# Kernel tuning notes

Hardware: AMD Instinct MI355X
Metric: run time of the kernel (lower is better)

## Reference

```python
import jax, jax.numpy as jnp
import numpy as np

B, C, H, W = 8, 64, 128, 128
OC, KH, KW = 64, 3, 3
STRIDE, PAD, DIL = 1, 1, 1
DG = 1            # deformable groups
G = 1             # conv groups
K = KH * KW
HO = (H + 2 * PAD - DIL * (KH - 1) - 1) // STRIDE + 1
WO = (W + 2 * PAD - DIL * (KW - 1) - 1) // STRIDE + 1


def setup_inputs() -> dict:
    key = jax.random.key(0)
    k1, k2, k3, k4 = jax.random.split(key, 4)
    input_tensor = jax.random.normal(k1, (B, C, H, W), dtype=jnp.float32)
    offset = jax.random.normal(k2, (B, DG * 2 * K, HO, WO), dtype=jnp.float32)
    mask = jax.random.uniform(k3, (B, DG * K, HO, WO), dtype=jnp.float32)
    n = C * KH * KW
    std_v = 1.0 / np.sqrt(n)
    weight = jax.random.uniform(k4, (OC, C // G, KH, KW), dtype=jnp.float32,
                                minval=-std_v, maxval=std_v)
    bias = jnp.zeros((OC,), dtype=jnp.float32)
    return {"input_tensor": input_tensor, "offset": offset, "mask": mask,
            "weight": weight, "bias": bias}


def _bilinear_sample(img, py, px):
    # img: [Cg, H, W]; py, px: [K, HO, WO] fractional sample coords
    y0 = jnp.floor(py).astype(jnp.int32)
    x0 = jnp.floor(px).astype(jnp.int32)
    y1, x1 = y0 + 1, x0 + 1
    wy1 = py - y0.astype(py.dtype)
    wx1 = px - x0.astype(px.dtype)
    wy0, wx0 = 1.0 - wy1, 1.0 - wx1

    def gather(yy, xx):
        valid = ((yy >= 0) & (yy < H) & (xx >= 0) & (xx < W)).astype(img.dtype)
        yc = jnp.clip(yy, 0, H - 1)
        xc = jnp.clip(xx, 0, W - 1)
        return img[:, yc, xc] * valid  # [Cg, K, HO, WO], zero outside

    return (gather(y0, x0) * (wy0 * wx0) + gather(y0, x1) * (wy0 * wx1)
            + gather(y1, x0) * (wy1 * wx0) + gather(y1, x1) * (wy1 * wx1))


def _mdconv(input_tensor, offset, mask, weight, bias):
    Cg = C // DG
    ky = (jnp.arange(K) // KW).astype(jnp.float32)   # kernel row per tap
    kx = (jnp.arange(K) % KW).astype(jnp.float32)    # kernel col per tap
    oy = jnp.arange(HO, dtype=jnp.float32) * STRIDE - PAD
    ox = jnp.arange(WO, dtype=jnp.float32) * STRIDE - PAD
    base_y = ky[:, None] * DIL + oy[None, :]         # [K, HO]
    base_x = kx[:, None] * DIL + ox[None, :]         # [K, WO]

    off = offset.reshape(B, DG, K, 2, HO, WO)
    py = base_y[None, None, :, :, None] + off[:, :, :, 0]  # [B, DG, K, HO, WO]
    px = base_x[None, None, :, None, :] + off[:, :, :, 1]

    imgs = input_tensor.reshape(B, DG, Cg, H, W)
    sample = jax.vmap(jax.vmap(_bilinear_sample))           # over B then DG
    cols = sample(imgs, py, px)                             # [B, DG, Cg, K, HO, WO]
    cols = cols * mask.reshape(B, DG, 1, K, HO, WO)
    cols = cols.reshape(B, G, C // G, K, HO, WO)

    w = weight.reshape(G, OC // G, C // G, K)
    out = jnp.einsum('gock,bgckpq->bgopq', w, cols)
    out = out.reshape(B, OC, HO, WO) + bias[None, :, None, None]
    return out


def reference(input_tensor, offset, mask, weight, bias):
    return _mdconv(input_tensor, offset, mask, weight, bias)
```

## Files before the change

### kernel.cpp

```cpp
#include <hip/hip_runtime.h>
#include <stdint.h>

typedef unsigned short u16;

#define B_ 8
#define C_ 64
#define H_ 128
#define W_ 128
#define OC_ 64
#define HO_ 128
#define WO_ 128
#define HWC_ (H_*W_*C_)
#define PADW 72

typedef __attribute__((ext_vector_type(8))) short short8;
typedef __attribute__((ext_vector_type(4))) float f32x4;

__device__ __forceinline__ u16 f2bf(float f) {
  union { float f; uint32_t i; } v; v.f = f;
  uint32_t r = v.i + 0x7FFFu + ((v.i >> 16) & 1u);
  return (u16)(r >> 16);
}
__device__ __forceinline__ uint32_t pkbf(float lo, float hi) {
  uint32_t r;
  asm("v_cvt_pk_bf16_f32 %0, %1, %2" : "=v"(r) : "v"(lo), "v"(hi));
  return r;
}
#define BF_LO(u) __uint_as_float((uint32_t)(u) << 16)
#define BF_HI(u) __uint_as_float((uint32_t)(u) & 0xFFFF0000u)

__global__ void wprep_kernel(const float* __restrict__ w, u16* __restrict__ wk2) {
  const int idx = blockIdx.x * 256 + threadIdx.x;
  const int j    = idx & 7;
  const int lane = (idx >> 3) & 63;
  const int kk   = (idx >> 9) & 1;
  const int m    = (idx >> 10) & 1;
  const int wr   = (idx >> 11) & 1;
  const int k    = idx >> 12;
  const int oc = wr*32 + m*16 + (lane & 15);
  const int c  = kk*32 + (lane >> 4)*8 + j;
  wk2[idx] = f2bf(w[(oc*C_ + c)*9 + k]);
}

__global__ __launch_bounds__(256) void nhwc_kernel(const float* __restrict__ in,
                                                   u16* __restrict__ nhwc) {
  __shared__ float t[64][65];
  const int b = blockIdx.z, h = blockIdx.y, w0 = blockIdx.x * 64;
  const int tid = threadIdx.x;
  for (int idx = tid; idx < 64*64; idx += 256) {
    int c = idx >> 6, w = idx & 63;
    t[w][c] = in[((b*C_ + c)*H_ + h)*W_ + w0 + w];
  }
  __syncthreads();
  for (int idx = tid; idx < 64*64; idx += 256) {
    int w = idx >> 6, c = idx & 63;
    nhwc[((b*H_ + h)*W_ + w0 + w)*C_ + c] = f2bf(t[w][c]);
  }
}

__device__ __forceinline__ uint32_t blend1(uint32_t g00, uint32_t g01,
                                           uint32_t g10, uint32_t g11, float4 w) {
  float lo = w.x*BF_LO(g00) + w.y*BF_LO(g01) + w.z*BF_LO(g10) + w.w*BF_LO(g11);
  float hi = w.x*BF_HI(g00) + w.y*BF_HI(g01) + w.z*BF_HI(g10) + w.w*BF_HI(g11);
  return pkbf(lo, hi);
}

__global__ __launch_bounds__(256, 4) void mdconv_main(
    const float* __restrict__ offs, const float* __restrict__ mask,
    const float* __restrict__ bias, const u16* __restrict__ nhwc,
    const u16* __restrict__ wk2, float* __restrict__ out)
{
  __shared__ u16 clds[64*PADW];
  __shared__ int2 pA[576];
  __shared__ float4 pW[576];

  const int tid = threadIdx.x;
  const int lane = tid & 63;
  const int wv = tid >> 6;
  const int b = blockIdx.z;
  const int p = blockIdx.y;
  const int q0 = blockIdx.x * 64;

  for (int item = tid; item < 576; item += 256) {
    const int k = item >> 6;
    const int px = item & 63;
    const int q = q0 + px;
    const int ky = k / 3, kx = k % 3;
    const float oy = offs[((b*18 + 2*k)*HO_ + p)*WO_ + q];
    const float ox = offs[((b*18 + 2*k + 1)*HO_ + p)*WO_ + q];
    const float mm = mask[((b*9 + k)*HO_ + p)*WO_ + q];
    const float py  = (float)(ky + p - 1) + oy;
    const float pxx = (float)(kx + q - 1) + ox;
    const float y0f = floorf(py), x0f = floorf(pxx);
    const int y0 = (int)y0f, x0 = (int)x0f;
    const int y1 = y0 + 1, x1 = x0 + 1;
    const float wy1 = py - y0f, wx1 = pxx - x0f;
    const float wy0 = 1.f - wy1, wx0 = 1.f - wx1;
    const bool vy0 = (y0 >= 0) & (y0 < H_);
    const bool vy1 = (y1 >= 0) & (y1 < H_);
    const bool vx0 = (x0 >= 0) & (x0 < W_);
    const bool vx1 = (x1 >= 0) & (x1 < W_);
    const float w00 = (vy0 & vx0) ? wy0*wx0*mm : 0.f;
    const float w01 = (vy0 & vx1) ? wy0*wx1*mm : 0.f;
    const float w10 = (vy1 & vx0) ? wy1*wx0*mm : 0.f;
    const float w11 = (vy1 & vx1) ? wy1*wx1*mm : 0.f;
    const int y0c = min(max(y0,0),H_-1), y1c = min(max(y1,0),H_-1);
    const int x0c = min(max(x0,0),W_-1), x1c = min(max(x1,0),W_-1);
    const int dx = (x1c - x0c) * C_;
    const int dy = (y1c - y0c) * W_ * C_;
    pA[item] = make_int2(b*HWC_ + (y0c*W_ + x0c)*C_, dx | (dy << 16));
    pW[item] = make_float4(w00, w01, w10, w11);
  }
  __syncthreads();

  f32x4 acc00 = {0.f,0.f,0.f,0.f};
  f32x4 acc01 = acc00, acc10 = acc00, acc11 = acc00;
  const int wr = wv >> 1, wc = wv & 1;
  const u16* cb = &clds[(wc*32 + (lane & 15))*PADW + (lane >> 4)*8];
  const int px0 = tid >> 3;
  const int c8 = (tid & 7) * 8;

  for (int k = 0; k < 9; ++k) {
    const u16* wg = wk2 + (k*2 + wr)*2048 + lane*8;
    const short8 a00 = *(const short8*)(wg);
    const short8 a01 = *(const short8*)(wg + 512);
    const short8 a10 = *(const short8*)(wg + 1024);
    const short8 a11 = *(const short8*)(wg + 1536);

    {
      const int piA = k*64 + px0, piB = piA + 32;
      const int2 aA = pA[piA];
      const int2 aB = pA[piB];
      const float4 wA = pW[piA];
      const float4 wB = pW[piB];
      const u16* sA = nhwc + aA.x + c8;
      const u16* sB = nhwc + aB.x + c8;
      const int dxA = aA.y & 0xFFFF, dyA = ((uint32_t)aA.y) >> 16;
      const int dxB = aB.y & 0xFFFF, dyB = ((uint32_t)aB.y) >> 16;
      const uint4 gA00 = *(const uint4*)(sA);
      const uint4 gA01 = *(const uint4*)(sA + dxA);
      const uint4 gA10 = *(const uint4*)(sA + dyA);
      const uint4 gA11 = *(const uint4*)(sA + dyA + dxA);
      const uint4 gB00 = *(const uint4*)(sB);
      const uint4 gB01 = *(const uint4*)(sB + dxB);
      const uint4 gB10 = *(const uint4*)(sB + dyB);
      const uint4 gB11 = *(const uint4*)(sB + dyB + dxB);
      uint4 rA, rB;
      rA.x = blend1(gA00.x, gA01.x, gA10.x, gA11.x, wA);
      rA.y = blend1(gA00.y, gA01.y, gA10.y, gA11.y, wA);
      rA.z = blend1(gA00.z, gA01.z, gA10.z, gA11.z, wA);
      rA.w = blend1(gA00.w, gA01.w, gA10.w, gA11.w, wA);
      rB.x = blend1(gB00.x, gB01.x, gB10.x, gB11.x, wB);
      rB.y = blend1(gB00.y, gB01.y, gB10.y, gB11.y, wB);
      rB.z = blend1(gB00.z, gB01.z, gB10.z, gB11.z, wB);
      rB.w = blend1(gB00.w, gB01.w, gB10.w, gB11.w, wB);
      *(uint4*)(&clds[px0*PADW + c8]) = rA;
      *(uint4*)(&clds[(px0+32)*PADW + c8]) = rB;
    }
    __syncthreads();

    const short8 b00 = *(const short8*)(cb);
    const short8 b01 = *(const short8*)(cb + 32);
    const short8 b10 = *(const short8*)(cb + 16*PADW);
    const short8 b11 = *(const short8*)(cb + 16*PADW + 32);
    acc00 = __builtin_amdgcn_mfma_f32_16x16x32_bf16(a00, b00, acc00, 0, 0, 0);
    acc00 = __builtin_amdgcn_mfma_f32_16x16x32_bf16(a01, b01, acc00, 0, 0, 0);
    acc01 = __builtin_amdgcn_mfma_f32_16x16x32_bf16(a00, b10, acc01, 0, 0, 0);
    acc01 = __builtin_amdgcn_mfma_f32_16x16x32_bf16(a01, b11, acc01, 0, 0, 0);
    acc10 = __builtin_amdgcn_mfma_f32_16x16x32_bf16(a10, b00, acc10, 0, 0, 0);
    acc10 = __builtin_amdgcn_mfma_f32_16x16x32_bf16(a11, b01, acc10, 0, 0, 0);
    acc11 = __builtin_amdgcn_mfma_f32_16x16x32_bf16(a10, b10, acc11, 0, 0, 0);
    acc11 = __builtin_amdgcn_mfma_f32_16x16x32_bf16(a11, b11, acc11, 0, 0, 0);
    if (k < 8) __syncthreads();
  }

  const int qc = q0 + wc*32 + (lane & 15);
  const int ocr = wr*32 + (lane >> 4)*4;
  #pragma unroll
  for (int m = 0; m < 2; ++m) {
    #pragma unroll
    for (int n = 0; n < 2; ++n) {
      const f32x4 a = (m==0) ? (n==0 ? acc00 : acc01) : (n==0 ? acc10 : acc11);
      #pragma unroll
      for (int j = 0; j < 4; ++j) {
        const int oc = ocr + m*16 + j;
        out[((b*OC_ + oc)*HO_ + p)*WO_ + qc + n*16] = a[j] + bias[oc];
      }
    }
  }
}

extern "C" void kernel_launch(void* const* d_in, const int* in_sizes, int n_in,
                              void* d_out, int out_size, void* d_ws, size_t ws_size,
                              hipStream_t stream) {
  const float* input  = (const float*)d_in[0];
  const float* offset = (const float*)d_in[1];
  const float* mask   = (const float*)d_in[2];
  const float* weight = (const float*)d_in[3];
  const float* bias   = (const float*)d_in[4];
  float* out = (float*)d_out;

  u16* nhwc = (u16*)d_ws;
  u16* wk2  = nhwc + (size_t)B_*H_*W_*C_;

  hipLaunchKernelGGL(wprep_kernel, dim3(144), dim3(256), 0, stream, weight, wk2);
  hipLaunchKernelGGL(nhwc_kernel, dim3(2, 128, 8), dim3(256), 0, stream, input, nhwc);
  hipLaunchKernelGGL(mdconv_main, dim3(2, 128, 8), dim3(256), 0, stream,
                     offset, mask, bias, nhwc, wk2, out);
}
```

Before: 60.36 us.

## Double-buffer column LDS tile and prefetch next tap's gathers during MFMA

```diff
diff --git a/kernel.cpp b/kernel.cpp
--- a/kernel.cpp
+++ b/kernel.cpp
@@ -70,7 +70,7 @@
     const float* __restrict__ bias, const u16* __restrict__ nhwc,
     const u16* __restrict__ wk2, float* __restrict__ out)
 {
-  __shared__ u16 clds[64*PADW];
+  __shared__ u16 clds[2][64*PADW];
   __shared__ int2 pA[576];
   __shared__ float4 pW[576];
 
@@ -116,49 +116,60 @@
   f32x4 acc00 = {0.f,0.f,0.f,0.f};
   f32x4 acc01 = acc00, acc10 = acc00, acc11 = acc00;
   const int wr = wv >> 1, wc = wv & 1;
-  const u16* cb = &clds[(wc*32 + (lane & 15))*PADW + (lane >> 4)*8];
   const int px0 = tid >> 3;
   const int c8 = (tid & 7) * 8;
 
+  short8 a00, a01, a10, a11;
+  short8 n00, n01, n10, n11;
+  uint4 gA00, gA01, gA10, gA11, gB00, gB01, gB10, gB11;
+  float4 wAx, wBx;
+
+#define GATHER(kk_) { \
+    const int piA = (kk_)*64 + px0, piB = piA + 32; \
+    const int2 aA = pA[piA]; const int2 aB = pA[piB]; \
+    wAx = pW[piA]; wBx = pW[piB]; \
+    const u16* sA = nhwc + aA.x + c8; \
+    const u16* sB = nhwc + aB.x + c8; \
+    const int dxA = aA.y & 0xFFFF, dyA = ((uint32_t)aA.y) >> 16; \
+    const int dxB = aB.y & 0xFFFF, dyB = ((uint32_t)aB.y) >> 16; \
+    gA00 = *(const uint4*)(sA);       gA01 = *(const uint4*)(sA + dxA); \
+    gA10 = *(const uint4*)(sA + dyA); gA11 = *(const uint4*)(sA + dyA + dxA); \
+    gB00 = *(const uint4*)(sB);       gB01 = *(const uint4*)(sB + dxB); \
+    gB10 = *(const uint4*)(sB + dyB); gB11 = *(const uint4*)(sB + dyB + dxB); }
+
+#define LOADA(kk_, d00, d01, d10, d11) { \
+    const u16* wg = wk2 + ((kk_)*2 + wr)*2048 + lane*8; \
+    d00 = *(const short8*)(wg);        d01 = *(const short8*)(wg + 512); \
+    d10 = *(const short8*)(wg + 1024); d11 = *(const short8*)(wg + 1536); }
+
+#define BLEND_WRITE(buf_) { \
+    uint4 rA, rB; \
+    rA.x = blend1(gA00.x, gA01.x, gA10.x, gA11.x, wAx); \
+    rA.y = blend1(gA00.y, gA01.y, gA10.y, gA11.y, wAx); \
+    rA.z = blend1(gA00.z, gA01.z, gA10.z, gA11.z, wAx); \
+    rA.w = blend1(gA00.w, gA01.w, gA10.w, gA11.w, wAx); \
+    rB.x = blend1(gB00.x, gB01.x, gB10.x, gB11.x, wBx); \
+    rB.y = blend1(gB00.y, gB01.y, gB10.y, gB11.y, wBx); \
+    rB.z = blend1(gB00.z, gB01.z, gB10.z, gB11.z, wBx); \
+    rB.w = blend1(gB00.w, gB01.w, gB10.w, gB11.w, wBx); \
+    *(uint4*)(&clds[buf_][px0*PADW + c8]) = rA; \
+    *(uint4*)(&clds[buf_][(px0+32)*PADW + c8]) = rB; }
+
+  GATHER(0);
+  LOADA(0, a00, a01, a10, a11);
+  BLEND_WRITE(0);
+  __syncthreads();
+
+  const u16* cb0 = &clds[0][(wc*32 + (lane & 15))*PADW + (lane >> 4)*8];
+  const u16* cb1 = &clds[1][(wc*32 + (lane & 15))*PADW + (lane >> 4)*8];
+
+#pragma unroll
   for (int k = 0; k < 9; ++k) {
-    const u16* wg = wk2 + (k*2 + wr)*2048 + lane*8;
-    const short8 a00 = *(const short8*)(wg);
-    const short8 a01 = *(const short8*)(wg + 512);
-    const short8 a10 = *(const short8*)(wg + 1024);
-    const short8 a11 = *(const short8*)(wg + 1536);
-
-    {
-      const int piA = k*64 + px0, piB = piA + 32;
-      const int2 aA = pA[piA];
-      const int2 aB = pA[piB];
-      const float4 wA = pW[piA];
-      const float4 wB = pW[piB];
-      const u16* sA = nhwc + aA.x + c8;
-      const u16* sB = nhwc + aB.x + c8;
-      const int dxA = aA.y & 0xFFFF, dyA = ((uint32_t)aA.y) >> 16;
-      const int dxB = aB.y & 0xFFFF, dyB = ((uint32_t)aB.y) >> 16;
-      const uint4 gA00 = *(const uint4*)(sA);
-      const uint4 gA01 = *(const uint4*)(sA + dxA);
-      const uint4 gA10 = *(const uint4*)(sA + dyA);
-      const uint4 gA11 = *(const uint4*)(sA + dyA + dxA);
-      const uint4 gB00 = *(const uint4*)(sB);
-      const uint4 gB01 = *(const uint4*)(sB + dxB);
-      const uint4 gB10 = *(const uint4*)(sB + dyB);
-      const uint4 gB11 = *(const uint4*)(sB + dyB + dxB);
-      uint4 rA, rB;
-      rA.x = blend1(gA00.x, gA01.x, gA10.x, gA11.x, wA);
-      rA.y = blend1(gA00.y, gA01.y, gA10.y, gA11.y, wA);
-      rA.z = blend1(gA00.z, gA01.z, gA10.z, gA11.z, wA);
-      rA.w = blend1(gA00.w, gA01.w, gA10.w, gA11.w, wA);
-      rB.x = blend1(gB00.x, gB01.x, gB10.x, gB11.x, wB);
-      rB.y = blend1(gB00.y, gB01.y, gB10.y, gB11.y, wB);
-      rB.z = blend1(gB00.z, gB01.z, gB10.z, gB11.z, wB);
-      rB.w = blend1(gB00.w, gB01.w, gB10.w, gB11.w, wB);
-      *(uint4*)(&clds[px0*PADW + c8]) = rA;
-      *(uint4*)(&clds[(px0+32)*PADW + c8]) = rB;
+    if (k < 8) {
+      GATHER(k+1);
+      LOADA(k+1, n00, n01, n10, n11);
     }
-    __syncthreads();
-
+    const u16* cb = (k & 1) ? cb1 : cb0;
     const short8 b00 = *(const short8*)(cb);
     const short8 b01 = *(const short8*)(cb + 32);
     const short8 b10 = *(const short8*)(cb + 16*PADW);
@@ -171,7 +182,11 @@
     acc10 = __builtin_amdgcn_mfma_f32_16x16x32_bf16(a11, b01, acc10, 0, 0, 0);
     acc11 = __builtin_amdgcn_mfma_f32_16x16x32_bf16(a10, b10, acc11, 0, 0, 0);
     acc11 = __builtin_amdgcn_mfma_f32_16x16x32_bf16(a11, b11, acc11, 0, 0, 0);
-    if (k < 8) __syncthreads();
+    if (k < 8) {
+      BLEND_WRITE((k+1) & 1);
+      __syncthreads();
+      a00 = n00; a01 = n01; a10 = n10; a11 = n11;
+    }
   }
 
   const int qc = q0 + wc*32 + (lane & 15);
```

Result: no change. 59.37 us (-1.6%).

## Give each wave a private gather tile, drop block barriers, pack blend math

Applied to the files above, without the earlier changes.

```diff
diff --git a/kernel.cpp b/kernel.cpp
--- a/kernel.cpp
+++ b/kernel.cpp
@@ -15,6 +15,7 @@
 
 typedef __attribute__((ext_vector_type(8))) short short8;
 typedef __attribute__((ext_vector_type(4))) float f32x4;
+typedef __attribute__((ext_vector_type(2))) float f32x2;
 
 __device__ __forceinline__ u16 f2bf(float f) {
   union { float f; uint32_t i; } v; v.f = f;
@@ -26,8 +27,17 @@
   asm("v_cvt_pk_bf16_f32 %0, %1, %2" : "=v"(r) : "v"(lo), "v"(hi));
   return r;
 }
-#define BF_LO(u) __uint_as_float((uint32_t)(u) << 16)
-#define BF_HI(u) __uint_as_float((uint32_t)(u) & 0xFFFF0000u)
+__device__ __forceinline__ f32x2 up2(uint32_t g) {
+  f32x2 r;
+  r.x = __uint_as_float(g << 16);
+  r.y = __uint_as_float(g & 0xFFFF0000u);
+  return r;
+}
+__device__ __forceinline__ uint32_t blend2(uint32_t g00, uint32_t g01,
+                                           uint32_t g10, uint32_t g11, float4 w) {
+  f32x2 s = up2(g00)*w.x + up2(g01)*w.y + up2(g10)*w.z + up2(g11)*w.w;
+  return pkbf(s.x, s.y);
+}
 
 __global__ void wprep_kernel(const float* __restrict__ w, u16* __restrict__ wk2) {
   const int idx = blockIdx.x * 256 + threadIdx.x;
@@ -58,19 +68,12 @@
   }
 }
 
-__device__ __forceinline__ uint32_t blend1(uint32_t g00, uint32_t g01,
-                                           uint32_t g10, uint32_t g11, float4 w) {
-  float lo = w.x*BF_LO(g00) + w.y*BF_LO(g01) + w.z*BF_LO(g10) + w.w*BF_LO(g11);
-  float hi = w.x*BF_HI(g00) + w.y*BF_HI(g01) + w.z*BF_HI(g10) + w.w*BF_HI(g11);
-  return pkbf(lo, hi);
-}
-
 __global__ __launch_bounds__(256, 4) void mdconv_main(
     const float* __restrict__ offs, const float* __restrict__ mask,
     const float* __restrict__ bias, const u16* __restrict__ nhwc,
     const u16* __restrict__ wk2, float* __restrict__ out)
 {
-  __shared__ u16 clds[64*PADW];
+  __shared__ u16 tlds[4][32*PADW];
   __shared__ int2 pA[576];
   __shared__ float4 pW[576];
 
@@ -116,10 +119,13 @@
   f32x4 acc00 = {0.f,0.f,0.f,0.f};
   f32x4 acc01 = acc00, acc10 = acc00, acc11 = acc00;
   const int wr = wv >> 1, wc = wv & 1;
-  const u16* cb = &clds[(wc*32 + (lane & 15))*PADW + (lane >> 4)*8];
-  const int px0 = tid >> 3;
-  const int c8 = (tid & 7) * 8;
-
+  const int pxg = lane >> 3;
+  const int c8  = (lane & 7) * 8;
+
+  u16* tw = &tlds[wv][0];
+  const u16* cb = &tlds[wv][(lane & 15)*PADW + (lane >> 4)*8];
+
+#pragma unroll
   for (int k = 0; k < 9; ++k) {
     const u16* wg = wk2 + (k*2 + wr)*2048 + lane*8;
     const short8 a00 = *(const short8*)(wg);
@@ -127,37 +133,29 @@
     const short8 a10 = *(const short8*)(wg + 1024);
     const short8 a11 = *(const short8*)(wg + 1536);
 
-    {
-      const int piA = k*64 + px0, piB = piA + 32;
-      const int2 aA = pA[piA];
-      const int2 aB = pA[piB];
-      const float4 wA = pW[piA];
-      const float4 wB = pW[piB];
-      const u16* sA = nhwc + aA.x + c8;
-      const u16* sB = nhwc + aB.x + c8;
-      const int dxA = aA.y & 0xFFFF, dyA = ((uint32_t)aA.y) >> 16;
-      const int dxB = aB.y & 0xFFFF, dyB = ((uint32_t)aB.y) >> 16;
-      const uint4 gA00 = *(const uint4*)(sA);
-      const uint4 gA01 = *(const uint4*)(sA + dxA);
-      const uint4 gA10 = *(const uint4*)(sA + dyA);
-      const uint4 gA11 = *(const uint4*)(sA + dyA + dxA);
-      const uint4 gB00 = *(const uint4*)(sB);
-      const uint4 gB01 = *(const uint4*)(sB + dxB);
-      const uint4 gB10 = *(const uint4*)(sB + dyB);
-      const uint4 gB11 = *(const uint4*)(sB + dyB + dxB);
-      uint4 rA, rB;
-      rA.x = blend1(gA00.x, gA01.x, gA10.x, gA11.x, wA);
-      rA.y = blend1(gA00.y, gA01.y, gA10.y, gA11.y, wA);
-      rA.z = blend1(gA00.z, gA01.z, gA10.z, gA11.z, wA);
-      rA.w = blend1(gA00.w, gA01.w, gA10.w, gA11.w, wA);
-      rB.x = blend1(gB00.x, gB01.x, gB10.x, gB11.x, wB);
-      rB.y = blend1(gB00.y, gB01.y, gB10.y, gB11.y, wB);
-      rB.z = blend1(gB00.z, gB01.z, gB10.z, gB11.z, wB);
-      rB.w = blend1(gB00.w, gB01.w, gB10.w, gB11.w, wB);
-      *(uint4*)(&clds[px0*PADW + c8]) = rA;
-      *(uint4*)(&clds[(px0+32)*PADW + c8]) = rB;
-    }
-    __syncthreads();
+    uint4 G0[4], G1[4], G2[4], G3[4];
+    float4 W0, W1, W2, W3;
+#define LOADG(g_, Gv, Wv) { \
+      const int pi = k*64 + wc*32 + (g_)*8 + pxg; \
+      const int2 aa = pA[pi]; Wv = pW[pi]; \
+      const u16* s = nhwc + aa.x + c8; \
+      const int dx = aa.y & 0xFFFF, dy = ((uint32_t)aa.y) >> 16; \
+      Gv[0] = *(const uint4*)(s); \
+      Gv[1] = *(const uint4*)(s + dx); \
+      Gv[2] = *(const uint4*)(s + dy); \
+      Gv[3] = *(const uint4*)(s + dy + dx); }
+    LOADG(0, G0, W0); LOADG(1, G1, W1); LOADG(2, G2, W2); LOADG(3, G3, W3);
+#undef LOADG
+
+#define BW(g_, Gv, Wv) { \
+      uint4 r; \
+      r.x = blend2(Gv[0].x, Gv[1].x, Gv[2].x, Gv[3].x, Wv); \
+      r.y = blend2(Gv[0].y, Gv[1].y, Gv[2].y, Gv[3].y, Wv); \
+      r.z = blend2(Gv[0].z, Gv[1].z, Gv[2].z, Gv[3].z, Wv); \
+      r.w = blend2(Gv[0].w, Gv[1].w, Gv[2].w, Gv[3].w, Wv); \
+      *(uint4*)(tw + ((g_)*8 + pxg)*PADW + c8) = r; }
+    BW(0, G0, W0); BW(1, G1, W1); BW(2, G2, W2); BW(3, G3, W3);
+#undef BW
 
     const short8 b00 = *(const short8*)(cb);
     const short8 b01 = *(const short8*)(cb + 32);
@@ -171,7 +169,6 @@
     acc10 = __builtin_amdgcn_mfma_f32_16x16x32_bf16(a11, b01, acc10, 0, 0, 0);
     acc11 = __builtin_amdgcn_mfma_f32_16x16x32_bf16(a10, b10, acc11, 0, 0, 0);
     acc11 = __builtin_amdgcn_mfma_f32_16x16x32_bf16(a11, b11, acc11, 0, 0, 0);
-    if (k < 8) __syncthreads();
   }
 
   const int qc = q0 + wc*32 + (lane & 15);
```

Measured after the change: 76.08 us. 26.0% more time.
